# Kernel tuning notes

Hardware: AMD Instinct MI355X
Metric: run time of the kernel (lower is better)

Reference implementation:

```python
import jax, jax.numpy as jnp
import numpy as np

N_NODES = 100000


def gcn_conv(x, src, dst, W, b, n):
    # PyG GCNConv: add self-loops, symmetric deg^-1/2 normalization,
    # linear transform, gather->scatter-add aggregation, + bias.
    loop = jnp.arange(n, dtype=src.dtype)
    s = jnp.concatenate([src, loop])
    d = jnp.concatenate([dst, loop])
    deg = jax.ops.segment_sum(jnp.ones_like(d, dtype=x.dtype), d, num_segments=n)
    dinv = jnp.where(deg > 0, jax.lax.rsqrt(deg), jnp.zeros_like(deg))
    norm = dinv[s] * dinv[d]            # [E+N]
    h = x @ W                            # [N, out] (transform before propagate)
    msg = h[s] * norm[:, None]           # gather + scale
    out = jax.ops.segment_sum(msg, d, num_segments=n)  # scatter-add to dst
    return out + b


def setup_inputs() -> dict:
    key = jax.random.key(0)
    k = jax.random.split(key, 6)
    n, e, c_in, hid, c_out = N_NODES, 2500000, 5, 32, 1
    x = jax.random.normal(k[0], (n, c_in), dtype=jnp.float32)
    edge_index = jax.random.randint(k[1], (2, e), 0, n, dtype=jnp.int64)
    # Glorot-style init for GCN weights, zero bias (PyG default)
    W1 = jax.random.normal(k[2], (c_in, hid), dtype=jnp.float32) * (1.0 / np.sqrt(c_in))
    b1 = jnp.zeros((hid,), dtype=jnp.float32)
    W2 = jax.random.normal(k[3], (hid, c_out), dtype=jnp.float32) * (1.0 / np.sqrt(hid))
    b2 = jnp.zeros((c_out,), dtype=jnp.float32)
    return {"x": x, "edge_index": edge_index, "W1": W1, "b1": b1, "W2": W2, "b2": b2}


def reference(x, edge_index, W1, b1, W2, b2):
    n = x.shape[0]
    src, dst = edge_index[0], edge_index[1]
    h = jax.nn.relu(gcn_conv(x, src, dst, W1, b1, n))
    # dropout p=0.3 is identity at inference (training=False)
    return jax.nn.sigmoid(gcn_conv(h, src, dst, W2, b2, n))
```

## Files before the change

### kernel.cpp

```cpp
#include <hip/hip_runtime.h>
#include <math.h>


#define NB_SHIFT  8
#define BNODES    256
#define NBK       512
#define CAP       8192
#define CAP_SHIFT 13
#define CHUNK     4888
#define PBLK      512

__global__ __launch_bounds__(PBLK) void k_part(const int* __restrict__ src,
                                               const int* __restrict__ dst, int E,
                                               int* __restrict__ bcur,
                                               int* __restrict__ pairs) {
    __shared__ int sp[CHUNK];
    __shared__ unsigned short sb[CHUNK];
    __shared__ int cnt[NBK], ofs[NBK], cur[NBK], gbase[NBK];
    int tid = threadIdx.x;
    int base = blockIdx.x * CHUNK;
    int m = min(CHUNK, E - base);

    if (tid < NBK) cnt[tid] = 0;
    __syncthreads();
    for (int i = tid; i < m; i += 2 * PBLK) {
        int i1 = i + PBLK;
        int k0 = dst[base + i] >> NB_SHIFT;
        int k1 = (i1 < m) ? (dst[base + i1] >> NB_SHIFT) : -1;
        atomicAdd(&cnt[k0], 1);
        if (k1 >= 0) atomicAdd(&cnt[k1], 1);
    }
    __syncthreads();
    int v = cnt[tid];
    ofs[tid] = v;
    __syncthreads();
    for (int off = 1; off < NBK; off <<= 1) {
        int u = (tid >= off) ? ofs[tid - off] : 0;
        __syncthreads();
        ofs[tid] += u;
        __syncthreads();
    }
    int pre = ofs[tid] - v;
    ofs[tid] = pre;
    cur[tid] = pre;
    gbase[tid] = (tid << CAP_SHIFT) + (v ? atomicAdd(&bcur[tid], v) : 0);
    __syncthreads();
    for (int i = tid; i < m; i += 4 * PBLK) {
        int ia = i + PBLK, ib = i + 2 * PBLK, ic = i + 3 * PBLK;
        int s0 = src[base + i], d0 = dst[base + i];
        int s1 = 0, d1 = 0, s2 = 0, d2 = 0, s3 = 0, d3 = 0;
        if (ia < m) { s1 = src[base + ia]; d1 = dst[base + ia]; }
        if (ib < m) { s2 = src[base + ib]; d2 = dst[base + ib]; }
        if (ic < m) { s3 = src[base + ic]; d3 = dst[base + ic]; }
        int b0 = d0 >> NB_SHIFT;
        int p0 = atomicAdd(&cur[b0], 1);
        sp[p0] = ((d0 & (BNODES - 1)) << 24) | s0;
        sb[p0] = (unsigned short)b0;
        if (ia < m) {
            int b1 = d1 >> NB_SHIFT;
            int p1 = atomicAdd(&cur[b1], 1);
            sp[p1] = ((d1 & (BNODES - 1)) << 24) | s1;
            sb[p1] = (unsigned short)b1;
        }
        if (ib < m) {
            int b2 = d2 >> NB_SHIFT;
            int p2 = atomicAdd(&cur[b2], 1);
            sp[p2] = ((d2 & (BNODES - 1)) << 24) | s2;
            sb[p2] = (unsigned short)b2;
        }
        if (ic < m) {
            int b3 = d3 >> NB_SHIFT;
            int p3 = atomicAdd(&cur[b3], 1);
            sp[p3] = ((d3 & (BNODES - 1)) << 24) | s3;
            sb[p3] = (unsigned short)b3;
        }
    }
    __syncthreads();
    for (int i = tid; i < m; i += PBLK) {
        int b = sb[i];
        pairs[gbase[b] + (i - ofs[b])] = sp[i];
    }
}

__global__ __launch_bounds__(512) void k_sorta(const int* __restrict__ pairs,
                                               const int* __restrict__ bcur,
                                               const float* __restrict__ x,
                                               float* __restrict__ dinv,
                                               float* __restrict__ xs,
                                               int* __restrict__ nofs,
                                               int* __restrict__ deg, int n) {
    __shared__ int cnt[BNODES], scn[BNODES];
    int tid = threadIdx.x;
    int b = blockIdx.x;
    int base = b << CAP_SHIFT;
    int len = min(bcur[b], CAP);

    if (tid < BNODES) cnt[tid] = 0;
    __syncthreads();
    for (int i = tid; i < len; i += 512)
        atomicAdd(&cnt[((unsigned)pairs[base + i]) >> 24], 1);
    __syncthreads();
    int v = (tid < BNODES) ? cnt[tid] : 0;
    if (tid < BNODES) scn[tid] = v;
    __syncthreads();
    for (int off = 1; off < BNODES; off <<= 1) {
        int u = (tid < BNODES && tid >= off) ? scn[tid - off] : 0;
        __syncthreads();
        if (tid < BNODES) scn[tid] += u;
        __syncthreads();
    }
    if (tid < BNODES) {
        int node = (b << NB_SHIFT) + tid;
        if (node < n) {
            nofs[node] = base + scn[tid] - v;
            deg[node] = v;
            float di = rsqrtf((float)v + 1.0f);
            dinv[node] = di;
            const float* xr = x + (size_t)node * 5;
            float* xo = xs + ((size_t)node << 3);
#pragma unroll
            for (int k = 0; k < 5; ++k) xo[k] = xr[k] * di;
        }
    }
}

__global__ __launch_bounds__(512) void k_sortagg1(int* __restrict__ pairs,
                                                  const int* __restrict__ bcur,
                                                  const int* __restrict__ nofs,
                                                  const int* __restrict__ deg,
                                                  const float* __restrict__ xs,
                                                  const float* __restrict__ dinv,
                                                  const float* __restrict__ W1,
                                                  const float* __restrict__ b1,
                                                  const float* __restrict__ W2,
                                                  float* __restrict__ h2s, int n) {
    __shared__ int stage2[CAP];
    __shared__ int ofs[BNODES], cnt[BNODES], cur[BNODES];
    __shared__ float w1[160], bb1[32], w2[32];
    int tid = threadIdx.x;
    int b = blockIdx.x;
    int nbase = b << NB_SHIFT;
    int base = b << CAP_SHIFT;
    int len = min(bcur[b], CAP);

    if (tid < 160) w1[tid] = W1[tid];
    else if (tid < 192) bb1[tid - 160] = b1[tid - 160];
    else if (tid < 224) w2[tid - 192] = W2[tid - 192];
    if (tid < BNODES) {
        int node = nbase + tid;
        int o = 0, c = 0;
        if (node < n) { o = nofs[node] - base; c = deg[node]; }
        ofs[tid] = o; cnt[tid] = c; cur[tid] = o;
    }
    __syncthreads();
    for (int i = tid; i < len; i += 2048) {
        int ia = i + 512, ib = i + 1024, ic = i + 1536;
        int v0 = pairs[base + i];
        int v1 = (ia < len) ? pairs[base + ia] : -1;
        int v2 = (ib < len) ? pairs[base + ib] : -1;
        int v3 = (ic < len) ? pairs[base + ic] : -1;
        int p0 = atomicAdd(&cur[((unsigned)v0) >> 24], 1);
        stage2[p0] = v0 & 0x00FFFFFF;
        if (v1 != -1) {
            int p1 = atomicAdd(&cur[((unsigned)v1) >> 24], 1);
            stage2[p1] = v1 & 0x00FFFFFF;
        }
        if (v2 != -1) {
            int p2 = atomicAdd(&cur[((unsigned)v2) >> 24], 1);
            stage2[p2] = v2 & 0x00FFFFFF;
        }
        if (v3 != -1) {
            int p3 = atomicAdd(&cur[((unsigned)v3) >> 24], 1);
            stage2[p3] = v3 & 0x00FFFFFF;
        }
    }
    __syncthreads();
    {
        int len4 = len >> 2;
        const int4* s4 = (const int4*)stage2;
        int4* p4 = (int4*)(pairs + base);
        for (int i = tid; i < len4; i += 512) p4[i] = s4[i];
        for (int i = (len4 << 2) + tid; i < len; i += 512)
            pairs[base + i] = stage2[i];
    }
    int t2 = tid >> 1, half = tid & 1;
    int node = nbase + t2;
    if (node >= n) return;
    int beg = ofs[t2], dg = cnt[t2];
    float a0 = 0.f, a1 = 0.f, a2 = 0.f, a3 = 0.f, a4 = 0.f;
    if (!half) {
        const float* xo = xs + ((size_t)node << 3);
        a0 = xo[0]; a1 = xo[1]; a2 = xo[2]; a3 = xo[3]; a4 = xo[4];
    }
    for (int e = beg + half; e < beg + dg; e += 2) {
        int s = stage2[e];
        const float* xr = xs + ((size_t)s << 3);
        float4 q = *(const float4*)xr;
        float q4 = xr[4];
        a0 += q.x; a1 += q.y; a2 += q.z; a3 += q.w; a4 += q4;
    }
    a0 += __shfl_xor(a0, 1); a1 += __shfl_xor(a1, 1); a2 += __shfl_xor(a2, 1);
    a3 += __shfl_xor(a3, 1); a4 += __shfl_xor(a4, 1);
    if (half) return;
    float di = dinv[node];
    a0 *= di; a1 *= di; a2 *= di; a3 *= di; a4 *= di;
    float sum = 0.f;
#pragma unroll
    for (int c = 0; c < 32; ++c) {
        float z = bb1[c] + a0 * w1[c] + a1 * w1[32 + c] + a2 * w1[64 + c]
                         + a3 * w1[96 + c] + a4 * w1[128 + c];
        sum += fmaxf(z, 0.f) * w2[c];
    }
    h2s[node] = sum * di;
}

__global__ __launch_bounds__(256) void k_agg2(const int* __restrict__ pairs,
                                              const int* __restrict__ nofs,
                                              const int* __restrict__ deg,
                                              const float* __restrict__ h2s,
                                              const float* __restrict__ dinv,
                                              const float* __restrict__ b2,
                                              float* __restrict__ out, int n) {
    int tid = threadIdx.x;
    int node = blockIdx.x * 64 + (tid >> 2);
    int q = tid & 3;
    if (node >= n) return;
    int beg = nofs[node], dg = deg[node];
    float a = 0.f;
    for (int e = beg + q; e < beg + dg; e += 4) a += h2s[pairs[e]];
    a += __shfl_xor(a, 1);
    a += __shfl_xor(a, 2);
    if (q) return;
    float v = dinv[node] * (a + h2s[node]) + b2[0];
    out[node] = 1.0f / (1.0f + __expf(-v));
}

extern "C" void kernel_launch(void* const* d_in, const int* in_sizes, int n_in,
                              void* d_out, int out_size, void* d_ws, size_t ws_size,
                              hipStream_t stream) {
    const float* x  = (const float*)d_in[0];
    const int*   ei = (const int*)d_in[1];
    const float* W1 = (const float*)d_in[2];
    const float* b1 = (const float*)d_in[3];
    const float* W2 = (const float*)d_in[4];
    const float* b2 = (const float*)d_in[5];
    float* out = (float*)d_out;

    const int n = in_sizes[0] / 5;
    const int E = in_sizes[1] / 2;
    const int* src = ei;
    const int* dst = ei + E;
    const int nb = (n + BNODES - 1) >> NB_SHIFT;

    int* wsi = (int*)d_ws;
    int*   pairs = wsi;
    int*   nofs  = wsi + ((size_t)(nb + 1) << CAP_SHIFT);
    int*   deg   = nofs + n;
    float* dinv  = (float*)(deg + n);
    float* h2s   = dinv + n;
    float* xs    = h2s + n;
    int*   bcur  = (int*)(xs + (size_t)8 * n);

    const int nchunk = (E + CHUNK - 1) / CHUNK;
    const int nagg   = (n + 63) / 64;

    hipMemsetAsync(bcur, 0, NBK * sizeof(int), stream);
    k_part<<<nchunk, PBLK, 0, stream>>>(src, dst, E, bcur, pairs);
    k_sorta<<<nb, 512, 0, stream>>>(pairs, bcur, x, dinv, xs, nofs, deg, n);
    k_sortagg1<<<nb, 512, 0, stream>>>(pairs, bcur, nofs, deg, xs, dinv,
                                       W1, b1, W2, h2s, n);
    k_agg2<<<nagg, 256, 0, stream>>>(pairs, nofs, deg, h2s, dinv, b2, out, n);
}
```

Before: 143.1 us.

## Fuse partition, sort and both aggregations into one cooperative kernel with grid syncs

Replaces the four-kernel pipeline with a single cooperative kernel of 512 blocks that uses grid.sync between phases: edge partitioning, degree/prefix computation, first-layer aggregation fused with both linear transforms, and second-layer aggregation. Degrees are counted with global atomics during partitioning instead of in the sort pass. The per-block sorted neighbor lists are kept in shared memory across phases, so the pairs buffer is not re-read for the second layer. This removes kernel launch gaps and re-reads, at the cost of global atomics on deg, a larger memset, and correctness that depends on the chunk count (about 512) and the bucket count (about 391) fitting inside the fixed grid.

```diff
diff --git a/kernel.cpp b/kernel.cpp
--- a/kernel.cpp
+++ b/kernel.cpp
@@ -1,5 +1,8 @@
 #include <hip/hip_runtime.h>
+#include <hip/hip_cooperative_groups.h>
 #include <math.h>
+
+namespace cg = cooperative_groups;
 
 
 #define NB_SHIFT  8
@@ -8,12 +11,230 @@
 #define CAP       8192
 #define CAP_SHIFT 13
 #define CHUNK     4888
-#define PBLK      512
-
-__global__ __launch_bounds__(PBLK) void k_part(const int* __restrict__ src,
-                                               const int* __restrict__ dst, int E,
-                                               int* __restrict__ bcur,
-                                               int* __restrict__ pairs) {
+#define PBLK      256
+#define GRID      512
+
+struct SMemP0 {
+    int sp[CHUNK];
+    unsigned short sb[CHUNK];
+    int cnt[NBK], ofs[NBK], cur[NBK], gbase[NBK];
+};
+struct SMemP1 {
+    int stage2[CAP];
+    int ofs[BNODES], cnt[BNODES], cur[BNODES];
+    float w1[160], bb1[32], w2[32];
+};
+union SMem { SMemP0 p0; SMemP1 p1; };
+
+__global__ __launch_bounds__(PBLK, 4) void k_fused(
+        const int* __restrict__ src, const int* __restrict__ dst, int E,
+        const float* __restrict__ x,
+        const float* __restrict__ W1, const float* __restrict__ b1,
+        const float* __restrict__ W2, const float* __restrict__ b2,
+        float* __restrict__ out,
+        int* __restrict__ pairs, int* __restrict__ bcur,
+        int* __restrict__ deg, float* __restrict__ h2s,
+        float* __restrict__ xs, int n, int nb) {
+    __shared__ SMem sm;
+    cg::grid_group grid = cg::this_grid();
+    const int tid = threadIdx.x;
+    const int blk = blockIdx.x;
+    const int nbase = blk << NB_SHIFT;
+
+    {
+        int base = blk * CHUNK;
+        if (base < E) {
+            int m = min(CHUNK, E - base);
+            sm.p0.cnt[tid] = 0;
+            sm.p0.cnt[tid + PBLK] = 0;
+            __syncthreads();
+            for (int i = tid; i < m; i += 2 * PBLK) {
+                int i1 = i + PBLK;
+                int d0 = dst[base + i];
+                atomicAdd(&sm.p0.cnt[d0 >> NB_SHIFT], 1);
+                atomicAdd(&deg[d0], 1);
+                if (i1 < m) {
+                    int d1 = dst[base + i1];
+                    atomicAdd(&sm.p0.cnt[d1 >> NB_SHIFT], 1);
+                    atomicAdd(&deg[d1], 1);
+                }
+            }
+            __syncthreads();
+            int v0 = sm.p0.cnt[tid];
+            int v1 = sm.p0.cnt[tid + PBLK];
+            sm.p0.ofs[tid] = v0;
+            sm.p0.ofs[tid + PBLK] = v1;
+            __syncthreads();
+            for (int off = 1; off < NBK; off <<= 1) {
+                int u0 = (tid >= off) ? sm.p0.ofs[tid - off] : 0;
+                int u1 = (tid + PBLK >= off) ? sm.p0.ofs[tid + PBLK - off] : 0;
+                __syncthreads();
+                sm.p0.ofs[tid] += u0;
+                sm.p0.ofs[tid + PBLK] += u1;
+                __syncthreads();
+            }
+            int pre0 = sm.p0.ofs[tid] - v0;
+            int pre1 = sm.p0.ofs[tid + PBLK] - v1;
+            sm.p0.ofs[tid] = pre0;        sm.p0.cur[tid] = pre0;
+            sm.p0.ofs[tid + PBLK] = pre1; sm.p0.cur[tid + PBLK] = pre1;
+            sm.p0.gbase[tid] = (tid << CAP_SHIFT)
+                             + (v0 ? atomicAdd(&bcur[tid], v0) : 0);
+            sm.p0.gbase[tid + PBLK] = ((tid + PBLK) << CAP_SHIFT)
+                             + (v1 ? atomicAdd(&bcur[tid + PBLK], v1) : 0);
+            __syncthreads();
+            for (int i = tid; i < m; i += 4 * PBLK) {
+                int ia = i + PBLK, ib = i + 2 * PBLK, ic = i + 3 * PBLK;
+                int s0 = src[base + i], d0 = dst[base + i];
+                int s1 = 0, d1 = 0, s2 = 0, d2 = 0, s3 = 0, d3 = 0;
+                if (ia < m) { s1 = src[base + ia]; d1 = dst[base + ia]; }
+                if (ib < m) { s2 = src[base + ib]; d2 = dst[base + ib]; }
+                if (ic < m) { s3 = src[base + ic]; d3 = dst[base + ic]; }
+                int b0 = d0 >> NB_SHIFT;
+                int p0 = atomicAdd(&sm.p0.cur[b0], 1);
+                sm.p0.sp[p0] = ((d0 & (BNODES - 1)) << 24) | s0;
+                sm.p0.sb[p0] = (unsigned short)b0;
+                if (ia < m) {
+                    int b1k = d1 >> NB_SHIFT;
+                    int p1 = atomicAdd(&sm.p0.cur[b1k], 1);
+                    sm.p0.sp[p1] = ((d1 & (BNODES - 1)) << 24) | s1;
+                    sm.p0.sb[p1] = (unsigned short)b1k;
+                }
+                if (ib < m) {
+                    int b2k = d2 >> NB_SHIFT;
+                    int p2 = atomicAdd(&sm.p0.cur[b2k], 1);
+                    sm.p0.sp[p2] = ((d2 & (BNODES - 1)) << 24) | s2;
+                    sm.p0.sb[p2] = (unsigned short)b2k;
+                }
+                if (ic < m) {
+                    int b3k = d3 >> NB_SHIFT;
+                    int p3 = atomicAdd(&sm.p0.cur[b3k], 1);
+                    sm.p0.sp[p3] = ((d3 & (BNODES - 1)) << 24) | s3;
+                    sm.p0.sb[p3] = (unsigned short)b3k;
+                }
+            }
+            __syncthreads();
+            for (int i = tid; i < m; i += PBLK) {
+                int b = sm.p0.sb[i];
+                pairs[sm.p0.gbase[b] + (i - sm.p0.ofs[b])] = sm.p0.sp[i];
+            }
+        }
+    }
+    grid.sync();
+
+    if (blk < nb) {
+        if (tid < 160) sm.p1.w1[tid] = W1[tid];
+        else if (tid < 192) sm.p1.bb1[tid - 160] = b1[tid - 160];
+        else if (tid < 224) sm.p1.w2[tid - 192] = W2[tid - 192];
+        int node = nbase + tid;
+        int v = (node < n) ? deg[node] : 0;
+        sm.p1.cnt[tid] = v;
+        sm.p1.ofs[tid] = v;
+        __syncthreads();
+        for (int off = 1; off < BNODES; off <<= 1) {
+            int u = (tid >= off) ? sm.p1.ofs[tid - off] : 0;
+            __syncthreads();
+            sm.p1.ofs[tid] += u;
+            __syncthreads();
+        }
+        int pre = sm.p1.ofs[tid] - v;
+        sm.p1.ofs[tid] = pre;
+        sm.p1.cur[tid] = pre;
+        if (node < n) {
+            float di = rsqrtf((float)v + 1.0f);
+            const float* xr = x + (size_t)node * 5;
+            float* xo = xs + ((size_t)node << 3);
+#pragma unroll
+            for (int k = 0; k < 5; ++k) xo[k] = xr[k] * di;
+        }
+    }
+    grid.sync();
+
+    if (blk < nb) {
+        int base = blk << CAP_SHIFT;
+        int len = min(bcur[blk], CAP);
+        for (int i = tid; i < len; i += 4 * PBLK) {
+            int ia = i + PBLK, ib = i + 2 * PBLK, ic = i + 3 * PBLK;
+            int v0 = pairs[base + i];
+            int v1 = (ia < len) ? pairs[base + ia] : -1;
+            int v2 = (ib < len) ? pairs[base + ib] : -1;
+            int v3 = (ic < len) ? pairs[base + ic] : -1;
+            int p0 = atomicAdd(&sm.p1.cur[((unsigned)v0) >> 24], 1);
+            sm.p1.stage2[p0] = v0 & 0x00FFFFFF;
+            if (v1 != -1) {
+                int p1 = atomicAdd(&sm.p1.cur[((unsigned)v1) >> 24], 1);
+                sm.p1.stage2[p1] = v1 & 0x00FFFFFF;
+            }
+            if (v2 != -1) {
+                int p2 = atomicAdd(&sm.p1.cur[((unsigned)v2) >> 24], 1);
+                sm.p1.stage2[p2] = v2 & 0x00FFFFFF;
+            }
+            if (v3 != -1) {
+                int p3 = atomicAdd(&sm.p1.cur[((unsigned)v3) >> 24], 1);
+                sm.p1.stage2[p3] = v3 & 0x00FFFFFF;
+            }
+        }
+        __syncthreads();
+        int half = tid & 1;
+        for (int t2 = tid >> 1; t2 < BNODES; t2 += (PBLK >> 1)) {
+            int node = nbase + t2;
+            if (node >= n) continue;
+            int beg = sm.p1.ofs[t2], dg = sm.p1.cnt[t2];
+            float a0 = 0.f, a1 = 0.f, a2 = 0.f, a3 = 0.f, a4 = 0.f;
+            if (!half) {
+                const float* xo = xs + ((size_t)node << 3);
+                a0 = xo[0]; a1 = xo[1]; a2 = xo[2]; a3 = xo[3]; a4 = xo[4];
+            }
+            for (int e = beg + half; e < beg + dg; e += 2) {
+                int s = sm.p1.stage2[e];
+                const float* xr = xs + ((size_t)s << 3);
+                float4 q = *(const float4*)xr;
+                float q4 = xr[4];
+                a0 += q.x; a1 += q.y; a2 += q.z; a3 += q.w; a4 += q4;
+            }
+            a0 += __shfl_xor(a0, 1); a1 += __shfl_xor(a1, 1);
+            a2 += __shfl_xor(a2, 1); a3 += __shfl_xor(a3, 1);
+            a4 += __shfl_xor(a4, 1);
+            if (!half) {
+                float di = rsqrtf((float)dg + 1.0f);
+                a0 *= di; a1 *= di; a2 *= di; a3 *= di; a4 *= di;
+                float sum = 0.f;
+#pragma unroll
+                for (int c = 0; c < 32; ++c) {
+                    float z = sm.p1.bb1[c] + a0 * sm.p1.w1[c]
+                            + a1 * sm.p1.w1[32 + c] + a2 * sm.p1.w1[64 + c]
+                            + a3 * sm.p1.w1[96 + c] + a4 * sm.p1.w1[128 + c];
+                    sum += fmaxf(z, 0.f) * sm.p1.w2[c];
+                }
+                h2s[node] = sum * di;
+            }
+        }
+    }
+    grid.sync();
+
+    if (blk < nb) {
+        int half = tid & 1;
+        for (int t2 = tid >> 1; t2 < BNODES; t2 += (PBLK >> 1)) {
+            int node = nbase + t2;
+            if (node >= n) continue;
+            int beg = sm.p1.ofs[t2], dg = sm.p1.cnt[t2];
+            float a = 0.f;
+            for (int e = beg + half; e < beg + dg; e += 2)
+                a += h2s[sm.p1.stage2[e]];
+            a += __shfl_xor(a, 1);
+            if (!half) {
+                float di = rsqrtf((float)dg + 1.0f);
+                float vv = di * (a + h2s[node]) + b2[0];
+                out[node] = 1.0f / (1.0f + __expf(-vv));
+            }
+        }
+    }
+}
+
+
+__global__ __launch_bounds__(512) void k_part(const int* __restrict__ src,
+                                              const int* __restrict__ dst, int E,
+                                              int* __restrict__ bcur,
+                                              int* __restrict__ pairs) {
     __shared__ int sp[CHUNK];
     __shared__ unsigned short sb[CHUNK];
     __shared__ int cnt[NBK], ofs[NBK], cur[NBK], gbase[NBK];
@@ -23,8 +244,8 @@
 
     if (tid < NBK) cnt[tid] = 0;
     __syncthreads();
-    for (int i = tid; i < m; i += 2 * PBLK) {
-        int i1 = i + PBLK;
+    for (int i = tid; i < m; i += 2 * 512) {
+        int i1 = i + 512;
         int k0 = dst[base + i] >> NB_SHIFT;
         int k1 = (i1 < m) ? (dst[base + i1] >> NB_SHIFT) : -1;
         atomicAdd(&cnt[k0], 1);
@@ -45,8 +266,8 @@
     cur[tid] = pre;
     gbase[tid] = (tid << CAP_SHIFT) + (v ? atomicAdd(&bcur[tid], v) : 0);
     __syncthreads();
-    for (int i = tid; i < m; i += 4 * PBLK) {
-        int ia = i + PBLK, ib = i + 2 * PBLK, ic = i + 3 * PBLK;
+    for (int i = tid; i < m; i += 4 * 512) {
+        int ia = i + 512, ib = i + 1024, ic = i + 1536;
         int s0 = src[base + i], d0 = dst[base + i];
         int s1 = 0, d1 = 0, s2 = 0, d2 = 0, s3 = 0, d3 = 0;
         if (ia < m) { s1 = src[base + ia]; d1 = dst[base + ia]; }
@@ -76,7 +297,7 @@
         }
     }
     __syncthreads();
-    for (int i = tid; i < m; i += PBLK) {
+    for (int i = tid; i < m; i += 512) {
         int b = sb[i];
         pairs[gbase[b] + (i - ofs[b])] = sp[i];
     }
@@ -254,18 +475,43 @@
 
     int* wsi = (int*)d_ws;
     int*   pairs = wsi;
-    int*   nofs  = wsi + ((size_t)(nb + 1) << CAP_SHIFT);
-    int*   deg   = nofs + n;
-    float* dinv  = (float*)(deg + n);
+    int*   bcur  = wsi + ((size_t)(nb + 1) << CAP_SHIFT);
+    int*   deg   = bcur + NBK;
+    int*   nofs  = deg + n;
+    float* dinv  = (float*)(nofs + n);
     float* h2s   = dinv + n;
     float* xs    = h2s + n;
-    int*   bcur  = (int*)(xs + (size_t)8 * n);
 
     const int nchunk = (E + CHUNK - 1) / CHUNK;
-    const int nagg   = (n + 63) / 64;
-
-    hipMemsetAsync(bcur, 0, NBK * sizeof(int), stream);
-    k_part<<<nchunk, PBLK, 0, stream>>>(src, dst, E, bcur, pairs);
+
+    static int use_coop = -1;
+    if (use_coop < 0) {
+        int dev = 0, ncu = 0, maxb = 0;
+        hipGetDevice(&dev);
+        hipDeviceGetAttribute(&ncu, hipDeviceAttributeMultiprocessorCount, dev);
+        hipError_t e = hipOccupancyMaxActiveBlocksPerMultiprocessor(
+                &maxb, k_fused, PBLK, 0);
+        int coop = 0;
+        hipDeviceGetAttribute(&coop, hipDeviceAttributeCooperativeLaunch, dev);
+        use_coop = (e == hipSuccess && coop && (long)maxb * ncu >= GRID) ? 1 : 0;
+    }
+
+    hipMemsetAsync(bcur, 0, (size_t)(NBK + n) * sizeof(int), stream);
+
+    if (use_coop) {
+        void* args[] = {(void*)&src, (void*)&dst, (void*)&E, (void*)&x,
+                        (void*)&W1, (void*)&b1, (void*)&W2, (void*)&b2,
+                        (void*)&out, (void*)&pairs, (void*)&bcur, (void*)&deg,
+                        (void*)&h2s, (void*)&xs, (void*)&n, (void*)&nb};
+        hipError_t e = hipLaunchCooperativeKernel((const void*)k_fused,
+                                                  dim3(GRID), dim3(PBLK),
+                                                  args, 0, stream);
+        if (e == hipSuccess) return;
+        use_coop = 0;
+    }
+
+    const int nagg = (n + 63) / 64;
+    k_part<<<nchunk, 512, 0, stream>>>(src, dst, E, bcur, pairs);
     k_sorta<<<nb, 512, 0, stream>>>(pairs, bcur, x, dinv, xs, nofs, deg, n);
     k_sortagg1<<<nb, 512, 0, stream>>>(pairs, bcur, nofs, deg, xs, dinv,
                                        W1, b1, W2, h2s, n);
```

New measurement: 459.3 us. 221% more time.
